# Optimization experiments

Measured on AMD Instinct MI355X. Metric: run time of the kernel, lower is better.

## Reference

```python
import jax, jax.numpy as jnp
import numpy as np

NUM_NODES = 16384
EMBED_DIM = 128
BATCH = 32


def setup_inputs() -> dict:
    key = jax.random.key(0)
    k1, k2, k3 = jax.random.split(key, 3)
    # xavier_uniform for embed_node: bound = sqrt(6/(fan_in+fan_out))
    xb = float(np.sqrt(6.0 / (NUM_NODES + EMBED_DIM)))
    embed_node = jax.random.uniform(k1, (NUM_NODES, EMBED_DIM), minval=-xb, maxval=xb, dtype=jnp.float32)
    # nn.Linear default init: U(-1/sqrt(fan_in), 1/sqrt(fan_in)). These params exist but
    # provably do not affect the output (root node at depth 0 is never updated).
    lb = float(np.sqrt(1.0 / EMBED_DIM))
    W_self = jax.random.uniform(k2, (EMBED_DIM, EMBED_DIM), minval=-lb, maxval=lb, dtype=jnp.float32)
    W_child = jax.random.uniform(k3, (EMBED_DIM, EMBED_DIM), minval=-lb, maxval=lb, dtype=jnp.float32)
    return {"embed_node": embed_node, "W_self": W_self, "W_child": W_child, "batch_size": BATCH}


def reference(embed_node, W_self, W_child, batch_size):
    # Faithful math of TreeBasedSpatialEmbedding.forward:
    # - adj_matrix_path=None -> tree_structures is None -> node_emb = embed_node.
    # - (Even with trees: depth-0 root is skipped in _tree_aggregate, so
    #   root_embedding[root_node] == embed_node[root_node]; identical result.)
    # Then: unsqueeze(0).expand(B,-1,-1) -> [B,N,D]; transpose(1,2) -> [B,D,N]; unsqueeze(-1) -> [B,D,N,1]
    n, d = embed_node.shape
    out = jnp.broadcast_to(embed_node.T[None, :, :], (batch_size, d, n))[..., None]
    return out
```

## Files before the change

kernel.cpp:

```cpp
#include <hip/hip_runtime.h>
#include <hip/hip_bf16.h>


#define NN 16384
#define DD 128
#define NB 32
#define CHUNK 2048

typedef float f4_t __attribute__((ext_vector_type(4)));

__global__ __launch_bounds__(256) void tree_embed_bcast_kernel(
    const float* __restrict__ E, float* __restrict__ out) {
    const int d  = blockIdx.x;
    const int n0 = blockIdx.y * CHUNK;
    const int t  = threadIdx.x;

    const float* e0 = E + (size_t)(n0 + (t << 2)) * DD + d;
    const float* e1 = e0 + (size_t)1024 * DD;
    f4_t va, vb;
    va.x = e0[0 * DD]; va.y = e0[1 * DD]; va.z = e0[2 * DD]; va.w = e0[3 * DD];
    vb.x = e1[0 * DD]; vb.y = e1[1 * DD]; vb.z = e1[2 * DD]; vb.w = e1[3 * DD];

    float* o = out + (size_t)d * NN + n0 + (t << 2);
    const size_t BSTRIDE = (size_t)DD * NN;
    #pragma unroll
    for (int b = 0; b < NB; ++b) {
        float* p = o + (size_t)b * BSTRIDE;
        *reinterpret_cast<f4_t*>(p) = va;
        *reinterpret_cast<f4_t*>(p + 1024) = vb;
    }
}

extern "C" void kernel_launch(void* const* d_in, const int* in_sizes, int n_in,
                              void* d_out, int out_size, void* d_ws, size_t ws_size,
                              hipStream_t stream) {
    const float* E = (const float*)d_in[0];
    float* out = (float*)d_out;
    dim3 grid(DD, NN / CHUNK);
    hipLaunchKernelGGL(tree_embed_bcast_kernel, grid, dim3(256), 0, stream,
                       E, out);
}
```

Baseline: 55.63 us.

## Transpose embedding tile through LDS and split the batch across blocks

Each block now loads an 8-column by 1024-row tile of the embedding with coalesced float4 reads and transposes it through padded shared memory. Each block then writes that tile for 8 batch copies, with the batch split across a third grid dimension. This replaces the strided scalar column reads with coalesced loads and gives every wave several independent float4 store streams. The costs are an LDS round trip, a barrier, each tile being reread four times (once per batch group), and float4 LDS reads that may be misaligned because of the +1 row padding.

```diff
diff --git a/kernel.cpp b/kernel.cpp
--- a/kernel.cpp
+++ b/kernel.cpp
@@ -5,29 +5,57 @@
 #define NN 16384
 #define DD 128
 #define NB 32
-#define CHUNK 2048
+#define DT 8
+#define NT 1024
+#define BT 8
 
 typedef float f4_t __attribute__((ext_vector_type(4)));
 
-__global__ __launch_bounds__(256) void tree_embed_bcast_kernel(
+__global__ __launch_bounds__(256) void tree_embed_kernel(
     const float* __restrict__ E, float* __restrict__ out) {
-    const int d  = blockIdx.x;
-    const int n0 = blockIdx.y * CHUNK;
-    const int t  = threadIdx.x;
+    __shared__ float lds[DT][NT + 1];
 
-    const float* e0 = E + (size_t)(n0 + (t << 2)) * DD + d;
-    const float* e1 = e0 + (size_t)1024 * DD;
-    f4_t va, vb;
-    va.x = e0[0 * DD]; va.y = e0[1 * DD]; va.z = e0[2 * DD]; va.w = e0[3 * DD];
-    vb.x = e1[0 * DD]; vb.y = e1[1 * DD]; vb.z = e1[2 * DD]; vb.w = e1[3 * DD];
+    const int d0 = blockIdx.x * DT;
+    const int n0 = blockIdx.y * NT;
+    const int b0 = blockIdx.z * BT;
+    const int tid = threadIdx.x;
 
-    float* o = out + (size_t)d * NN + n0 + (t << 2);
+    {
+        const int c = tid & 1;
+        const int nl0 = tid >> 1;
+        #pragma unroll
+        for (int i = 0; i < NT / 128; ++i) {
+            const int n = nl0 + (i << 7);
+            const f4_t v = *reinterpret_cast<const f4_t*>(
+                &E[(size_t)(n0 + n) * DD + d0 + (c << 2)]);
+            lds[(c << 2) + 0][n] = v.x;
+            lds[(c << 2) + 1][n] = v.y;
+            lds[(c << 2) + 2][n] = v.z;
+            lds[(c << 2) + 3][n] = v.w;
+        }
+    }
+    __syncthreads();
+
+    const int l = tid & 63;
+    const int w = tid >> 6;
     const size_t BSTRIDE = (size_t)DD * NN;
     #pragma unroll
-    for (int b = 0; b < NB; ++b) {
-        float* p = o + (size_t)b * BSTRIDE;
-        *reinterpret_cast<f4_t*>(p) = va;
-        *reinterpret_cast<f4_t*>(p + 1024) = vb;
+    for (int r = 0; r < DT / 4; ++r) {
+        const int d = (r << 2) + w;
+        const int nb = l << 2;
+        const f4_t v0 = *reinterpret_cast<const f4_t*>(&lds[d][nb]);
+        const f4_t v1 = *reinterpret_cast<const f4_t*>(&lds[d][nb + 256]);
+        const f4_t v2 = *reinterpret_cast<const f4_t*>(&lds[d][nb + 512]);
+        const f4_t v3 = *reinterpret_cast<const f4_t*>(&lds[d][nb + 768]);
+        float* obase = out + (size_t)(d0 + d) * NN + n0 + nb;
+        #pragma unroll
+        for (int b = 0; b < BT; ++b) {
+            float* p = obase + (size_t)(b0 + b) * BSTRIDE;
+            *reinterpret_cast<f4_t*>(p)       = v0;
+            *reinterpret_cast<f4_t*>(p + 256) = v1;
+            *reinterpret_cast<f4_t*>(p + 512) = v2;
+            *reinterpret_cast<f4_t*>(p + 768) = v3;
+        }
     }
 }
 
@@ -36,7 +64,6 @@
                               hipStream_t stream) {
     const float* E = (const float*)d_in[0];
     float* out = (float*)d_out;
-    dim3 grid(DD, NN / CHUNK);
-    hipLaunchKernelGGL(tree_embed_bcast_kernel, grid, dim3(256), 0, stream,
-                       E, out);
+    dim3 grid(DD / DT, NN / NT, NB / BT);
+    hipLaunchKernelGGL(tree_embed_kernel, grid, dim3(256), 0, stream, E, out);
 }
```

Measured after the change: 56.57 us. Within noise of the previous version (+1.7%).
